# Performance work log

Measured on AMD Instinct MI355X. Metric: run time of the kernel, lower is better.

The kernel has to match this reference:

```python
import jax, jax.numpy as jnp
import numpy as np

N_QUAT = 4
VERONESE_DIM = 10
OUT_FEATURES = 132

# static index sets matching torch.triu_indices(4, 4)
_rows, _cols = np.triu_indices(N_QUAT)          # 10 upper-tri entries
_mask = _rows != _cols
TRIU_ROWS = jnp.asarray(_rows)
TRIU_COLS = jnp.asarray(_cols)
SYM_ROWS = jnp.asarray(_cols[_mask])            # mirrored lower-tri
SYM_COLS = jnp.asarray(_rows[_mask])
SYM_Z_IDX = jnp.asarray(np.nonzero(_mask)[0])


def setup_inputs() -> dict:
    key = jax.random.key(0)
    k_z, k_w1, k_w2 = jax.random.split(key, 3)
    B, D_IN, D_HID, D_OUT_NN = 65536, 256, 1024, 128
    z = jax.random.normal(k_z, (B, D_IN), dtype=jnp.float32)
    W1 = jax.random.normal(k_w1, (D_IN, D_HID), dtype=jnp.float32) * 0.02
    b1 = jnp.zeros((D_HID,), dtype=jnp.float32)
    W2 = jax.random.normal(k_w2, (D_HID, D_OUT_NN), dtype=jnp.float32) * 0.02
    b2 = jnp.zeros((D_OUT_NN,), dtype=jnp.float32)
    return {"z": z, "W1": W1, "b1": b1, "W2": W2, "b2": b2}


def _recover_quat(z_v):
    # z_v: (B, 10) -> symmetric (B, 4, 4) -> top eigenvector -> (B, 4)
    B = z_v.shape[0]
    M = jnp.zeros((B, N_QUAT, N_QUAT), dtype=z_v.dtype)
    M = M.at[:, TRIU_ROWS, TRIU_COLS].set(z_v)
    M = M.at[:, SYM_ROWS, SYM_COLS].set(z_v[:, SYM_Z_IDX])
    _, vecs = jnp.linalg.eigh(M)          # eigenvalues ascending
    q = vecs[:, :, -1]                    # eigenvector of largest eigenvalue
    sign = jnp.sign(q[:, 0:1] + 1e-9)
    return q * sign


def reference(z, W1, b1, W2, b2):
    orig_shape = z.shape
    zf = z.reshape(-1, orig_shape[-1])           # (B, in_features)
    q_pred = _recover_quat(zf[:, :VERONESE_DIM])  # (B, 4)
    h = jax.nn.relu(zf @ W1 + b1)
    others = h @ W2 + b2                          # (B, 128)
    B = zf.shape[0]
    out = jnp.zeros((B, OUT_FEATURES), dtype=zf.dtype)
    out = out.at[:, :N_QUAT].set(q_pred)          # quat_indices = [0,1,2,3]
    out = out.at[:, N_QUAT:].set(others)          # non_quat = [4..131]
    return out.reshape(*orig_shape[:-1], OUT_FEATURES)
```

## Files before the change

kernel.cpp:

```cpp
#include <hip/hip_runtime.h>


typedef short s16x8 __attribute__((ext_vector_type(8)));
typedef float f32x4 __attribute__((ext_vector_type(4)));
typedef float f32x16 __attribute__((ext_vector_type(16)));
typedef unsigned char u8;

__device__ __forceinline__ f32x16 mfma32(s16x8 a, s16x8 b, f32x16 c) {
    return __builtin_amdgcn_mfma_f32_32x32x16_bf16(a, b, c, 0, 0, 0);
}

__device__ __forceinline__ short f2bf(float f) {
    unsigned int u = __float_as_uint(f);
    u = (u + 0x7fffu + ((u >> 16) & 1u)) >> 16;
    return (short)u;
}

__device__ __forceinline__ unsigned cvt_pk(float lo, float hi) {
    unsigned r;
    asm("v_cvt_pk_bf16_f32 %0, %1, %2" : "=v"(r) : "v"(lo), "v"(hi));
    return r;
}

__device__ __forceinline__ void pl32swap(unsigned& a, unsigned& b) {
    asm("v_permlane32_swap_b32 %0, %1" : "+v"(a), "+v"(b));
}

__device__ __forceinline__ void gload_lds16(const void* g, void* l) {
    __builtin_amdgcn_global_load_lds(
        (const __attribute__((address_space(1))) unsigned int*)g,
        (__attribute__((address_space(3))) unsigned int*)l, 16, 0, 0);
}

__global__ __launch_bounds__(256) void prep_weights(
    const float* __restrict__ W1, const float* __restrict__ W2,
    uint4* __restrict__ w1t, uint4* __restrict__ w2t)
{
    int tid = blockIdx.x * 256 + threadIdx.x;
    int hl = (tid >> 5) & 1, r32 = tid & 31;
    union { short b[8]; uint4 v; } pk;
    if (tid < 32768) {
        int s  = (tid >> 6) & 15;
        int ct = (tid >> 10) & 1;
        int c  = tid >> 11;
        int k0 = s * 16 + hl * 8;
        int n1 = c * 64 + ct * 32 + r32;
        #pragma unroll
        for (int j = 0; j < 8; ++j)
            pk.b[j] = f2bf(W1[(k0 + j) * 1024 + n1]);
        w1t[tid] = pk.v;
    } else {
        int g  = tid - 32768;
        int nt = (g >> 6) & 3;
        int K  = g >> 8;
        int k0 = K * 16 + hl * 8;
        int n2 = nt * 32 + r32;
        #pragma unroll
        for (int j = 0; j < 8; ++j)
            pk.b[j] = f2bf(W2[(k0 + j) * 128 + n2]);
        w2t[g] = pk.v;
    }
}

__global__ __launch_bounds__(512, 1) void fused_all(
    const float* __restrict__ z, const float* __restrict__ b1,
    const float* __restrict__ b2, const uint4* __restrict__ w1t,
    const uint4* __restrict__ w2t, float* __restrict__ out)
{
    __shared__ __align__(16) u8 lds[135168];

    const int t    = threadIdx.x;
    const int lane = t & 63;
    const int w    = t >> 6;
    const int hl   = lane >> 5;
    const int r32  = lane & 31;
    const int bm0  = blockIdx.x * 256;
    const int rowbase = bm0 + w * 32;

    #pragma unroll
    for (int i = 0; i < 8; ++i) {
        int f = i * 512 + t;
        gload_lds16(w1t + f, lds + f * 16);
    }
    if (t < 256) gload_lds16(b1 + t * 4, lds + 131072 + t * 16);

    if (lane < 32) {
        int row = rowbase + lane;
        const float* zr = z + (size_t)row * 256;
        float4 v0 = *(const float4*)(zr);
        float4 v1 = *(const float4*)(zr + 4);
        float2 v2 = *(const float2*)(zr + 8);

        float A[4][4] = {{v0.x, v0.y, v0.z, v0.w},
                         {v0.y, v1.x, v1.y, v1.z},
                         {v0.z, v1.y, v1.w, v2.x},
                         {v0.w, v1.z, v2.x, v2.y}};
        float V[4][4] = {{1.f, 0.f, 0.f, 0.f},
                         {0.f, 1.f, 0.f, 0.f},
                         {0.f, 0.f, 1.f, 0.f},
                         {0.f, 0.f, 0.f, 1.f}};

#define ROT(p, qq) do {                                                   \
        float apq  = A[p][qq];                                            \
        float tau  = (A[qq][qq] - A[p][p]) *                              \
                     __builtin_amdgcn_rcpf(2.0f * apq);                   \
        float tt   = __builtin_amdgcn_rcpf(                               \
                        fabsf(tau) +                                      \
                        __builtin_amdgcn_sqrtf(fmaf(tau, tau, 1.0f)));    \
        tt = copysignf(tt, tau);                                          \
        tt = (fabsf(apq) > 1e-20f) ? tt : 0.0f;                           \
        float cth = __builtin_amdgcn_rsqf(fmaf(tt, tt, 1.0f));            \
        float sth = tt * cth;                                             \
        _Pragma("unroll")                                                 \
        for (int k = 0; k < 4; ++k) {                                     \
            float akp = A[k][p], akq = A[k][qq];                          \
            A[k][p]  = cth * akp - sth * akq;                             \
            A[k][qq] = sth * akp + cth * akq;                             \
        }                                                                 \
        _Pragma("unroll")                                                 \
        for (int k = 0; k < 4; ++k) {                                     \
            float apk = A[p][k], aqk = A[qq][k];                          \
            A[p][k]  = cth * apk - sth * aqk;                             \
            A[qq][k] = sth * apk + cth * aqk;                             \
        }                                                                 \
        _Pragma("unroll")                                                 \
        for (int k = 0; k < 4; ++k) {                                     \
            float vkp = V[k][p], vkq = V[k][qq];                          \
            V[k][p]  = cth * vkp - sth * vkq;                             \
            V[k][qq] = sth * vkp + cth * vkq;                             \
        }                                                                 \
    } while (0)

        #pragma unroll 1
        for (int sweep = 0; sweep < 6; ++sweep) {
            ROT(0, 1); ROT(0, 2); ROT(0, 3); ROT(1, 2); ROT(1, 3); ROT(2, 3);
        }
#undef ROT

        float bv = A[0][0];
        float q0 = V[0][0], q1 = V[1][0], q2 = V[2][0], q3 = V[3][0];
        #pragma unroll
        for (int k = 1; k < 4; ++k) {
            bool better = A[k][k] > bv;
            bv = better ? A[k][k] : bv;
            q0 = better ? V[0][k] : q0;
            q1 = better ? V[1][k] : q1;
            q2 = better ? V[2][k] : q2;
            q3 = better ? V[3][k] : q3;
        }
        float sgn = (q0 + 1e-9f) >= 0.0f ? 1.0f : -1.0f;
        *(float4*)(out + (size_t)row * 132) =
            make_float4(sgn * q0, sgn * q1, sgn * q2, sgn * q3);
    }

    s16x8 zf[16];
    {
        const float* zp = z + (size_t)(rowbase + r32) * 256 + hl * 8;
        #pragma unroll
        for (int s = 0; s < 16; ++s) {
            float4 a0 = *(const float4*)(zp + s * 16);
            float4 a1 = *(const float4*)(zp + s * 16 + 4);
            union { unsigned u[4]; s16x8 v; } pk;
            pk.u[0] = cvt_pk(a0.x, a0.y);
            pk.u[1] = cvt_pk(a0.z, a0.w);
            pk.u[2] = cvt_pk(a1.x, a1.y);
            pk.u[3] = cvt_pk(a1.z, a1.w);
            zf[s] = pk.v;
        }
    }

    const f32x16 zero16 = {0.f,0.f,0.f,0.f, 0.f,0.f,0.f,0.f,
                           0.f,0.f,0.f,0.f, 0.f,0.f,0.f,0.f};
    f32x16 acc2[4];
    #pragma unroll
    for (int nt = 0; nt < 4; ++nt) acc2[nt] = zero16;

    __syncthreads();

    const u8* const aA0 = lds +          lane * 16;
    const u8* const aA1 = lds + 32768  + lane * 16;
    const u8* const aB0 = lds + 65536  + lane * 16;
    const u8* const aB1 = lds + 98304  + lane * 16;
    u8* const sA = lds;
    u8* const sB = lds + 65536;
    const u8* const blsp = lds + 131072 + hl * 16;
    const s16x8* const w2b = (const s16x8*)w2t + lane;

    auto pack = [&](const f32x16& d, const u8* bb, int ct, s16x8* hfo) {
        unsigned Plo[4], Phi[4];
        #pragma unroll
        for (int g = 0; g < 4; ++g) {
            f32x4 bv = *(const f32x4*)(bb + ct * 128 + g * 32);
            Plo[g] = cvt_pk(fmaxf(d[4*g+0] + bv[0], 0.f),
                            fmaxf(d[4*g+1] + bv[1], 0.f));
            Phi[g] = cvt_pk(fmaxf(d[4*g+2] + bv[2], 0.f),
                            fmaxf(d[4*g+3] + bv[3], 0.f));
        }
        #pragma unroll
        for (int f = 0; f < 2; ++f) {
            unsigned a0 = Plo[2*f], b0 = Plo[2*f+1];
            unsigned a1 = Phi[2*f], b1_ = Phi[2*f+1];
            pl32swap(a0, b0);
            pl32swap(a1, b1_);
            union { unsigned u[4]; s16x8 v; } fr;
            fr.u[0] = a0; fr.u[1] = a1; fr.u[2] = b0; fr.u[3] = b1_;
            hfo[f] = fr.v;
        }
    };

    auto body = [&](int c, const u8* a) {
        const s16x8* w2c = w2b + c * 1024;
        s16x8 w2f[4][4];
        #pragma unroll
        for (int ks = 0; ks < 4; ++ks)
            #pragma unroll
            for (int nt = 0; nt < 4; ++nt)
                w2f[ks][nt] = w2c[(ks * 4 + nt) * 64];

        const u8* bb = blsp + c * 256;
        s16x8 hf[4];

        __builtin_amdgcn_s_setprio(1);
        f32x16 d0 = zero16, d1 = zero16;
        #pragma unroll
        for (int s = 0; s < 16; ++s) {
            s16x8 a0 = *(const s16x8*)(a + s * 1024);
            s16x8 a1 = *(const s16x8*)(a + (16 + s) * 1024);
            d0 = mfma32(a0, zf[s], d0);
            d1 = mfma32(a1, zf[s], d1);
        }
        __builtin_amdgcn_s_setprio(0);

        pack(d0, bb, 0, hf);
        pack(d1, bb, 1, hf + 2);

        __builtin_amdgcn_s_setprio(1);
        #pragma unroll
        for (int ks = 0; ks < 4; ++ks)
            #pragma unroll
            for (int nt = 0; nt < 4; ++nt)
                acc2[nt] = mfma32(hf[ks], w2f[ks][nt], acc2[nt]);
        __builtin_amdgcn_s_setprio(0);
    };

    auto group = [&](int g, const u8* a0, const u8* a1, u8* dst, bool LASTG) {
        if (!LASTG) {
            const uint4* s1 = w1t + (2 * g + 2) * 2048;
            #pragma unroll
            for (int i = 0; i < 8; ++i) {
                int f = i * 512 + t;
                gload_lds16(s1 + f, dst + f * 16);
            }
        }
        body(2 * g,     a0);
        body(2 * g + 1, a1);
        __syncthreads();
    };

    #pragma unroll 1
    for (int gg = 0; gg < 4; ++gg) {
        group(2 * gg,     aA0, aA1, sB, false);
        group(2 * gg + 1, aB0, aB1, sA, gg == 3);
    }

    #pragma unroll
    for (int nt = 0; nt < 4; ++nt) {
        const float b2v = b2[nt * 32 + r32];
        #pragma unroll
        for (int r = 0; r < 16; ++r) {
            int m = (r & 3) + 8 * (r >> 2) + 4 * hl;
            out[(size_t)(rowbase + m) * 132 + 4 + nt * 32 + r32] =
                acc2[nt][r] + b2v;
        }
    }
}

extern "C" void kernel_launch(void* const* d_in, const int* in_sizes, int n_in,
                              void* d_out, int out_size, void* d_ws, size_t ws_size,
                              hipStream_t stream) {
    const float* z  = (const float*)d_in[0];
    const float* W1 = (const float*)d_in[1];
    const float* b1 = (const float*)d_in[2];
    const float* W2 = (const float*)d_in[3];
    const float* b2 = (const float*)d_in[4];
    float* out = (float*)d_out;

    uint4* w1t = (uint4*)d_ws;
    uint4* w2t = (uint4*)((char*)d_ws + 512 * 1024);

    hipLaunchKernelGGL(prep_weights, dim3(192), dim3(256), 0, stream,
                       W1, W2, w1t, w2t);
    hipLaunchKernelGGL(fused_all, dim3(256), dim3(512), 0, stream,
                       z, b1, b2, (const uint4*)w1t, (const uint4*)w2t, out);
}
```

Before: 72.90 us.

## Triple-buffer W1/W2 chunks in LDS with fine-grained phased barriers

Restages the main loop as a fully unrolled 16-chunk pipeline with three LDS buffers, each holding both a W1 and a W2 chunk. W2 fragments now come from LDS instead of per-wave global loads, and W2 prep is re-laid out per chunk to match. Each chunk is split into six phases: LDS fragments are loaded, a slice of the next-next chunk's global-to-LDS copy is issued, and MFMAs run between barriers with explicit vmcnt/lgkmcnt waits. The aim is to hide global latency and remove redundant W2 global traffic, at the cost of many more barriers, more LDS, and a much larger unrolled body.

```diff
diff --git a/kernel.cpp b/kernel.cpp
--- a/kernel.cpp
+++ b/kernel.cpp
@@ -31,6 +31,10 @@
         (const __attribute__((address_space(1))) unsigned int*)g,
         (__attribute__((address_space(3))) unsigned int*)l, 16, 0, 0);
 }
+
+#define BARRIER() __builtin_amdgcn_s_barrier()
+#define LGKM0()   do { asm volatile("s_waitcnt lgkmcnt(0)" ::: "memory"); \
+                       __builtin_amdgcn_sched_barrier(0); } while (0)
 
 __global__ __launch_bounds__(256) void prep_weights(
     const float* __restrict__ W1, const float* __restrict__ W2,
@@ -52,8 +56,9 @@
     } else {
         int g  = tid - 32768;
         int nt = (g >> 6) & 3;
-        int K  = g >> 8;
-        int k0 = K * 16 + hl * 8;
+        int ks = (g >> 8) & 3;
+        int c  = g >> 10;
+        int k0 = c * 64 + ks * 16 + hl * 8;
         int n2 = nt * 32 + r32;
         #pragma unroll
         for (int j = 0; j < 8; ++j)
@@ -67,7 +72,7 @@
     const float* __restrict__ b2, const uint4* __restrict__ w1t,
     const uint4* __restrict__ w2t, float* __restrict__ out)
 {
-    __shared__ __align__(16) u8 lds[135168];
+    __shared__ __align__(16) u8 lds[151552];
 
     const int t    = threadIdx.x;
     const int lane = t & 63;
@@ -78,11 +83,18 @@
     const int rowbase = bm0 + w * 32;
 
     #pragma unroll
-    for (int i = 0; i < 8; ++i) {
+    for (int i = 0; i < 4; ++i) {
         int f = i * 512 + t;
         gload_lds16(w1t + f, lds + f * 16);
-    }
-    if (t < 256) gload_lds16(b1 + t * 4, lds + 131072 + t * 16);
+        gload_lds16(w1t + 2048 + f, lds + 49152 + f * 16);
+    }
+    #pragma unroll
+    for (int i = 0; i < 2; ++i) {
+        int f = i * 512 + t;
+        gload_lds16(w2t + f, lds + 32768 + f * 16);
+        gload_lds16(w2t + 1024 + f, lds + 49152 + 32768 + f * 16);
+    }
+    if (t < 256) gload_lds16(b1 + t * 4, lds + 147456 + t * 16);
 
     if (lane < 32) {
         int row = rowbase + lane;
@@ -177,14 +189,15 @@
 
     __syncthreads();
 
-    const u8* const aA0 = lds +          lane * 16;
-    const u8* const aA1 = lds + 32768  + lane * 16;
-    const u8* const aB0 = lds + 65536  + lane * 16;
-    const u8* const aB1 = lds + 98304  + lane * 16;
-    u8* const sA = lds;
-    u8* const sB = lds + 65536;
-    const u8* const blsp = lds + 131072 + hl * 16;
-    const s16x8* const w2b = (const s16x8*)w2t + lane;
+    const u8* const bufp0 = lds +          lane * 16;
+    const u8* const bufp1 = lds + 49152  + lane * 16;
+    const u8* const bufp2 = lds + 98304  + lane * 16;
+    const u8* const blsp  = lds + 147456 + hl * 16;
+    u8* const bufs0 = lds;
+    u8* const bufs1 = lds + 49152;
+    u8* const bufs2 = lds + 98304;
+
+    s16x8 hf[4];
 
     auto pack = [&](const f32x16& d, const u8* bb, int ct, s16x8* hfo) {
         unsigned Plo[4], Phi[4];
@@ -208,59 +221,118 @@
         }
     };
 
-    auto body = [&](int c, const u8* a) {
-        const s16x8* w2c = w2b + c * 1024;
-        s16x8 w2f[4][4];
-        #pragma unroll
-        for (int ks = 0; ks < 4; ++ks)
-            #pragma unroll
-            for (int nt = 0; nt < 4; ++nt)
-                w2f[ks][nt] = w2c[(ks * 4 + nt) * 64];
-
+    #pragma unroll
+    for (int c = 0; c < 16; ++c) {
+        const int ci = c % 3;
+        const u8* a  = (ci == 0) ? bufp0 : (ci == 1) ? bufp1 : bufp2;
+        const u8* wf = a + 32768;
+        const int di = (c + 2) % 3;
+        u8* dst = (di == 0) ? bufs0 : (di == 1) ? bufs1 : bufs2;
+        const uint4* s1 = w1t + (c + 2) * 2048;
+        const uint4* s2 = w2t + (c + 2) * 1024;
+        const bool ST = (c <= 13);
         const u8* bb = blsp + c * 256;
-        s16x8 hf[4];
-
-        __builtin_amdgcn_s_setprio(1);
+
+        if (c >= 2) {
+            if (c <= 14) asm volatile("s_waitcnt vmcnt(6)" ::: "memory");
+            else         asm volatile("s_waitcnt vmcnt(0)" ::: "memory");
+            __builtin_amdgcn_sched_barrier(0);
+        }
+
         f32x16 d0 = zero16, d1 = zero16;
-        #pragma unroll
-        for (int s = 0; s < 16; ++s) {
-            s16x8 a0 = *(const s16x8*)(a + s * 1024);
-            s16x8 a1 = *(const s16x8*)(a + (16 + s) * 1024);
-            d0 = mfma32(a0, zf[s], d0);
-            d1 = mfma32(a1, zf[s], d1);
-        }
-        __builtin_amdgcn_s_setprio(0);
-
-        pack(d0, bb, 0, hf);
-        pack(d1, bb, 1, hf + 2);
-
-        __builtin_amdgcn_s_setprio(1);
-        #pragma unroll
-        for (int ks = 0; ks < 4; ++ks)
-            #pragma unroll
-            for (int nt = 0; nt < 4; ++nt)
-                acc2[nt] = mfma32(hf[ks], w2f[ks][nt], acc2[nt]);
-        __builtin_amdgcn_s_setprio(0);
-    };
-
-    auto group = [&](int g, const u8* a0, const u8* a1, u8* dst, bool LASTG) {
-        if (!LASTG) {
-            const uint4* s1 = w1t + (2 * g + 2) * 2048;
-            #pragma unroll
-            for (int i = 0; i < 8; ++i) {
-                int f = i * 512 + t;
-                gload_lds16(s1 + f, dst + f * 16);
+
+        {
+            s16x8 af[8];
+            #pragma unroll
+            for (int s = 0; s < 8; ++s)
+                af[s] = *(const s16x8*)(a + s * 1024);
+            if (ST) {
+                gload_lds16(s1 + t,       dst + t * 16);
+                gload_lds16(s1 + 512 + t, dst + 8192 + t * 16);
             }
-        }
-        body(2 * g,     a0);
-        body(2 * g + 1, a1);
-        __syncthreads();
-    };
-
-    #pragma unroll 1
-    for (int gg = 0; gg < 4; ++gg) {
-        group(2 * gg,     aA0, aA1, sB, false);
-        group(2 * gg + 1, aB0, aB1, sA, gg == 3);
+            BARRIER(); LGKM0();
+            __builtin_amdgcn_s_setprio(1);
+            #pragma unroll
+            for (int s = 0; s < 8; ++s) d0 = mfma32(af[s], zf[s], d0);
+            __builtin_amdgcn_s_setprio(0);
+            BARRIER();
+        }
+        {
+            s16x8 af[8];
+            #pragma unroll
+            for (int s = 0; s < 8; ++s)
+                af[s] = *(const s16x8*)(a + (8 + s) * 1024);
+            if (ST) {
+                gload_lds16(s1 + 1024 + t, dst + 16384 + t * 16);
+                gload_lds16(s1 + 1536 + t, dst + 24576 + t * 16);
+            }
+            BARRIER(); LGKM0();
+            __builtin_amdgcn_s_setprio(1);
+            #pragma unroll
+            for (int s = 0; s < 8; ++s) d0 = mfma32(af[s], zf[8 + s], d0);
+            __builtin_amdgcn_s_setprio(0);
+            BARRIER();
+        }
+        {
+            s16x8 af[8];
+            #pragma unroll
+            for (int s = 0; s < 8; ++s)
+                af[s] = *(const s16x8*)(a + (16 + s) * 1024);
+            if (ST) {
+                gload_lds16(s2 + t,       dst + 32768 + t * 16);
+                gload_lds16(s2 + 512 + t, dst + 40960 + t * 16);
+            }
+            BARRIER(); LGKM0();
+            __builtin_amdgcn_s_setprio(1);
+            #pragma unroll
+            for (int s = 0; s < 8; ++s) d1 = mfma32(af[s], zf[s], d1);
+            __builtin_amdgcn_s_setprio(0);
+            BARRIER();
+        }
+        {
+            s16x8 af[8];
+            #pragma unroll
+            for (int s = 0; s < 8; ++s)
+                af[s] = *(const s16x8*)(a + (24 + s) * 1024);
+            BARRIER(); LGKM0();
+            __builtin_amdgcn_s_setprio(1);
+            #pragma unroll
+            for (int s = 0; s < 8; ++s) d1 = mfma32(af[s], zf[8 + s], d1);
+            __builtin_amdgcn_s_setprio(0);
+            BARRIER();
+        }
+        {
+            s16x8 wfr[8];
+            #pragma unroll
+            for (int i = 0; i < 8; ++i)
+                wfr[i] = *(const s16x8*)(wf + i * 1024);
+            pack(d0, bb, 0, hf);
+            BARRIER(); LGKM0();
+            __builtin_amdgcn_s_setprio(1);
+            #pragma unroll
+            for (int ks = 0; ks < 2; ++ks)
+                #pragma unroll
+                for (int nt = 0; nt < 4; ++nt)
+                    acc2[nt] = mfma32(hf[ks], wfr[ks * 4 + nt], acc2[nt]);
+            __builtin_amdgcn_s_setprio(0);
+            BARRIER();
+        }
+        {
+            s16x8 wfr[8];
+            #pragma unroll
+            for (int i = 0; i < 8; ++i)
+                wfr[i] = *(const s16x8*)(wf + (8 + i) * 1024);
+            pack(d1, bb, 1, hf + 2);
+            BARRIER(); LGKM0();
+            __builtin_amdgcn_s_setprio(1);
+            #pragma unroll
+            for (int ks = 0; ks < 2; ++ks)
+                #pragma unroll
+                for (int nt = 0; nt < 4; ++nt)
+                    acc2[nt] = mfma32(hf[2 + ks], wfr[ks * 4 + nt], acc2[nt]);
+            __builtin_amdgcn_s_setprio(0);
+            BARRIER();
+        }
     }
 
     #pragma unroll
```

New measurement: 71.77 us. Within noise of the previous version (-1.6%).
